# Optimization experiments

Measured on AMD Instinct MI355X. Metric: run time of the kernel, lower is better.

Reference implementation:

```python
import jax, jax.numpy as jnp
import numpy as np

B, S, D, H = 2, 2048, 1024, 16
DH = D // H  # head dim = 64


def _split_heads(x):
    # [B,S,D] -> [B,H,S,DH]
    return x.reshape(B, S, H, DH).transpose(0, 2, 1, 3)


def setup_inputs() -> dict:
    key = jax.random.key(0)
    ks = jax.random.split(key, 14)
    sc = 1.0 / np.sqrt(D)
    p = {"hidden_states": jax.random.normal(ks[0], (B, S, D), jnp.float32)}
    names = ["Wq", "Wk1", "Wk2", "Wv1", "Wv2", "Wd"]
    for i, n in enumerate(names):
        p[n] = jax.random.normal(ks[1 + 2 * i], (D, D), jnp.float32) * sc
        p["b" + n[1:]] = jax.random.normal(ks[2 + 2 * i], (D,), jnp.float32) * 0.02
    return p


def reference(hidden_states, Wq, bq, Wk1, bk1, Wk2, bk2, Wv1, bv1, Wv2, bv2, Wd, bd):
    q = _split_heads(hidden_states @ Wq + bq)
    k1 = _split_heads(hidden_states @ Wk1 + bk1)
    k2 = _split_heads(hidden_states @ Wk2 + bk2)
    v1 = _split_heads(hidden_states @ Wv1 + bv1)
    v2 = _split_heads(hidden_states @ Wv2 + bv2)

    scores = jnp.einsum("bhqd,bhkd->bhqk", q, k1) / np.sqrt(DH)
    causal = jnp.tril(jnp.ones((S, S), dtype=bool))  # True = keep
    scores = jnp.where(causal, scores, -jnp.inf)
    probs = jax.nn.softmax(scores, axis=-1)

    ctx = jnp.einsum("bhqk,bhkd->bhqd", probs, v1)          # [B,H,S,DH]
    ctx = jnp.einsum("bhqd,bhkd->bhqk", ctx, k2)            # [B,H,S,S]
    ctx = jnp.einsum("bhqk,bhkd->bhqd", ctx, v2)            # [B,H,S,DH]

    ctx = ctx.transpose(0, 2, 1, 3).reshape(B, S, D)
    return ctx @ Wd + bd
```

## Files before the change

### kernel.cpp

```cpp
#include <hip/hip_runtime.h>
#include <hip/hip_bf16.h>

typedef __bf16 bf16x8 __attribute__((ext_vector_type(8)));
typedef float f32x4 __attribute__((ext_vector_type(4)));
using bf16 = __hip_bfloat16;

#define SEQ 2048
#define DM 1024
#define NH 16
#define DH 64
#define NBH 32
#define MR 4096

#define WAITBAR(N) asm volatile("s_waitcnt vmcnt(" #N ")\n\ts_barrier" ::: "memory")

static __device__ __forceinline__ void async_cp16(const void* gsrc, void* ldsdst) {
  __builtin_amdgcn_global_load_lds((__attribute__((address_space(1))) void*)gsrc,
                                   (__attribute__((address_space(3))) void*)ldsdst, 16, 0, 0);
}

static __device__ __forceinline__ unsigned short f2bfu(float f) {
  bf16 h = __float2bfloat16(f);
  unsigned short u; __builtin_memcpy(&u, &h, 2); return u;
}
static __device__ __forceinline__ unsigned int pack_bf2(float lo, float hi) {
  return (unsigned int)f2bfu(lo) | ((unsigned int)f2bfu(hi) << 16);
}

struct WPtrs { const float* w[6]; };

__global__ __launch_bounds__(256) void prep(WPtrs wp, const float* __restrict__ X,
                                            bf16* __restrict__ WtAll, bf16* __restrict__ Xb,
                                            float* __restrict__ Mb) {
  __shared__ float Ts[32][33];
  const int z = blockIdx.z;
  const int tid = threadIdx.x;
  if (z < 6) {
    const float* W = wp.w[z];
    bf16* Wt = WtAll + (long)z * DM * DM;
    const int n0 = blockIdx.x * 32, k0 = blockIdx.y * 32;
    const int tx = tid & 31, ty = tid >> 5;
#pragma unroll
    for (int it = 0; it < 4; ++it)
      Ts[ty + 8 * it][tx] = W[(long)(k0 + ty + 8 * it) * DM + n0 + tx];
    __syncthreads();
#pragma unroll
    for (int it = 0; it < 4; ++it)
      Wt[(long)(n0 + ty + 8 * it) * DM + k0 + tx] = __float2bfloat16(Ts[tx][ty + 8 * it]);
    if (z == 0 && tid < 32) {
      int lin = blockIdx.x + 32 * blockIdx.y;
      f32x4 zz = {0.f, 0.f, 0.f, 0.f};
      *(f32x4*)(Mb + lin * 128 + tid * 4) = zz;
    }
  } else {
    int lin = blockIdx.x + 32 * blockIdx.y + (z - 6) * 1024;
    long g = (long)lin * 2048 + tid * 8;
    float4 a = *(const float4*)(X + g);
    float4 b = *(const float4*)(X + g + 4);
    unsigned short u[8];
    u[0]=f2bfu(a.x); u[1]=f2bfu(a.y); u[2]=f2bfu(a.z); u[3]=f2bfu(a.w);
    u[4]=f2bfu(b.x); u[5]=f2bfu(b.y); u[6]=f2bfu(b.z); u[7]=f2bfu(b.w);
    uint4 o; __builtin_memcpy(&o, u, 16);
    *(uint4*)(Xb + g) = o;
  }
}

struct ProjArgs {
  const float* bias[5];
  bf16* out[5];
};

__global__ __launch_bounds__(256, 2) void gemm_proj(const bf16* __restrict__ A,
                                                    const bf16* __restrict__ WtAll, ProjArgs p) {
  __shared__ alignas(16) bf16 SM[36864];
  bf16* As = SM;
  bf16* Bs = SM + 12288;
  const int tid = threadIdx.x;
  const int bid = blockIdx.x;
  const int wave = tid >> 6, lane = tid & 63, l15 = lane & 15, l4 = lane >> 4;
  const int wm = wave >> 1, wn = wave & 1;
  const int slot8 = (l4 ^ ((l15 >> 1) & 3)) * 8;
  const int prow = tid >> 2;
  const int cc = (tid & 3) ^ ((prow >> 1) & 3);
  char* dA = (char*)As + wave * 1024;
  char* dB = (char*)Bs + wave * 1024;

  if (bid < 512) {
    const int mt = bid & 31, nt = bid >> 5;
    const int m0 = mt * 128;
    const int z = nt >> 2;
    const int n0z = (nt & 3) * 256;
    const bf16* Bt = WtAll + (long)z * DM * DM + (long)n0z * DM;

    const bf16* sA0 = A  + (long)(m0 + prow) * DM + cc * 8;
    const bf16* sA1 = sA0 + 64L * DM;
    const bf16* sB0 = Bt + (long)prow * DM + cc * 8;
    const bf16* sB1 = sB0 + 64L * DM;
    const bf16* sB2 = sB0 + 128L * DM;
    const bf16* sB3 = sB0 + 192L * DM;

#define PSTAGE(KT_, BUF_) do {                                  \
    int ko_ = (KT_) * 32;                                       \
    async_cp16(sA0 + ko_, dA + (BUF_) * 8192);                  \
    async_cp16(sA1 + ko_, dA + (BUF_) * 8192 + 4096);           \
    async_cp16(sB0 + ko_, dB + (BUF_) * 16384);                 \
    async_cp16(sB1 + ko_, dB + (BUF_) * 16384 + 4096);          \
    async_cp16(sB2 + ko_, dB + (BUF_) * 16384 + 8192);          \
    async_cp16(sB3 + ko_, dB + (BUF_) * 16384 + 12288);         \
  } while (0)

    const int arow = wm * 64 + l15;
    const int brow = wn * 128 + l15;
    f32x4 acc[4][8] = {};

#define PCOMPUTE(BUF_) do {                                                        \
    const bf16* ab_ = As + (BUF_) * 4096;                                          \
    const bf16* bb_ = Bs + (BUF_) * 8192;                                          \
    bf16x8 af_[4], bq_[8];                                                         \
    _Pragma("unroll")                                                              \
    for (int i = 0; i < 4; ++i) af_[i] = *(const bf16x8*)(ab_ + (arow + i * 16) * 32 + slot8); \
    _Pragma("unroll")                                                              \
    for (int j = 0; j < 8; ++j) bq_[j] = *(const bf16x8*)(bb_ + (brow + j * 16) * 32 + slot8); \
    _Pragma("unroll")                                                              \
    for (int i = 0; i < 4; ++i)                                                    \
      _Pragma("unroll")                                                            \
      for (int j = 0; j < 8; ++j)                                                  \
        acc[i][j] = __builtin_amdgcn_mfma_f32_16x16x32_bf16(af_[i], bq_[j], acc[i][j], 0, 0, 0); \
  } while (0)

    PSTAGE(0, 0);
    PSTAGE(1, 1);
    int buf = 0;
#pragma unroll 1
    for (int k = 0; k < 31; ++k) {
      WAITBAR(6);
      if (k < 30) {
        int nb = buf + 2; if (nb > 2) nb -= 3;
        PSTAGE(k + 2, nb);
      }
      PCOMPUTE(buf);
      ++buf; if (buf > 2) buf = 0;
    }
    WAITBAR(0);
    PCOMPUTE(buf);
#undef PSTAGE
#undef PCOMPUTE

    const float* bias = p.bias[z];
    bf16* out = p.out[z];
    float bv[8];
#pragma unroll
    for (int j = 0; j < 8; ++j) bv[j] = bias[n0z + wn * 128 + j * 16 + l15];

    if (z < 2) {
      const float scale = (z == 0) ? 0.125f * 1.44269504f : 1.0f;
#pragma unroll
      for (int i = 0; i < 4; ++i)
#pragma unroll
        for (int j = 0; j < 8; ++j)
#pragma unroll
          for (int r = 0; r < 4; ++r) {
            int m = m0 + wm * 64 + i * 16 + l4 * 4 + r;
            int n = n0z + wn * 128 + j * 16 + l15;
            int b = m >> 11, s = m & 2047, hh = n >> 6, d = n & 63;
            out[((long)((b * NH + hh) * SEQ + s)) * DH + d] =
                __float2bfloat16((acc[i][j][r] + bv[j]) * scale);
          }
    } else {
      __syncthreads();
      bf16* Os = SM;
#pragma unroll
      for (int i = 0; i < 4; ++i)
#pragma unroll
        for (int j = 0; j < 8; ++j)
#pragma unroll
          for (int r = 0; r < 4; ++r) {
            int nl = wn * 128 + j * 16 + l15;
            int ml = wm * 64 + i * 16 + l4 * 4 + r;
            Os[nl * 136 + ml] = __float2bfloat16(acc[i][j][r] + bv[j]);
          }
      __syncthreads();
      {
        int nl = tid;
        int ng = n0z + nl;
        int hh = ng >> 6, d = ng & 63;
        int b = m0 >> 11, s0 = m0 & 2047;
        bf16* op = out + ((long)((b * NH + hh) * DH + d)) * SEQ + s0;
#pragma unroll
        for (int u = 0; u < 16; ++u)
          *(bf16x8*)(op + u * 8) = *(const bf16x8*)(Os + nl * 136 + u * 8);
      }
    }
  } else {
    const int tb = bid - 512;
    const int mt = tb & 31, nt16 = tb >> 5;
    const int m0 = mt * 128, n0 = nt16 * 64;
    const bf16* Bt = WtAll + 4L * DM * DM + (long)n0 * DM;

    const bf16* sA0 = A + (long)(m0 + prow) * DM + cc * 8;
    const bf16* sA1 = sA0 + 64L * DM;
    const bf16* sB0 = Bt + (long)prow * DM + cc * 8;

#define TSTAGE(KT_, BUF_) do {                                  \
    int ko_ = (KT_) * 32;                                       \
    async_cp16(sA0 + ko_, dA + (BUF_) * 8192);                  \
    async_cp16(sA1 + ko_, dA + (BUF_) * 8192 + 4096);           \
    async_cp16(sB0 + ko_, dB + (BUF_) * 4096);                  \
  } while (0)

    const int arow = wm * 64 + l15;
    const int brow = wn * 32 + l15;
    f32x4 acc2[4][2] = {};

#define TCOMPUTE(BUF_) do {                                                        \
    const bf16* ab_ = As + (BUF_) * 4096;                                          \
    const bf16* bb_ = Bs + (BUF_) * 2048;                                          \
    bf16x8 af_[4], bq_[2];                                                         \
    _Pragma("unroll")                                                              \
    for (int i = 0; i < 4; ++i) af_[i] = *(const bf16x8*)(ab_ + (arow + i * 16) * 32 + slot8); \
    _Pragma("unroll")                                                              \
    for (int j = 0; j < 2; ++j) bq_[j] = *(const bf16x8*)(bb_ + (brow + j * 16) * 32 + slot8); \
    _Pragma("unroll")                                                              \
    for (int i = 0; i < 4; ++i)                                                    \
      _Pragma("unroll")                                                            \
      for (int j = 0; j < 2; ++j)                                                  \
        acc2[i][j] = __builtin_amdgcn_mfma_f32_16x16x32_bf16(af_[i], bq_[j], acc2[i][j], 0, 0, 0); \
  } while (0)

    TSTAGE(0, 0);
    TSTAGE(1, 1);
    int buf = 0;
#pragma unroll 1
    for (int k = 0; k < 31; ++k) {
      WAITBAR(3);
      if (k < 30) {
        int nb = buf + 2; if (nb > 2) nb -= 3;
        TSTAGE(k + 2, nb);
      }
      TCOMPUTE(buf);
      ++buf; if (buf > 2) buf = 0;
    }
    WAITBAR(0);
    TCOMPUTE(buf);
#undef TSTAGE
#undef TCOMPUTE

    float bv2[2];
#pragma unroll
    for (int j = 0; j < 2; ++j) bv2[j] = p.bias[4][n0 + wn * 32 + j * 16 + l15];
    __syncthreads();
    bf16* Os = SM;
#pragma unroll
    for (int i = 0; i < 4; ++i)
#pragma unroll
      for (int j = 0; j < 2; ++j)
#pragma unroll
        for (int r = 0; r < 4; ++r) {
          int nl = wn * 32 + j * 16 + l15;
          int ml = wm * 64 + i * 16 + l4 * 4 + r;
          Os[nl * 136 + ml] = __float2bfloat16(acc2[i][j][r] + bv2[j]);
        }
    __syncthreads();
    {
      int nl = tid & 63, seg = tid >> 6;
      int ng = n0 + nl;
      int hh = ng >> 6, d = ng & 63;
      int b = m0 >> 11, s0 = m0 & 2047;
      bf16* op = p.out[4] + ((long)((b * NH + hh) * DH + d)) * SEQ + s0 + seg * 32;
#pragma unroll
      for (int u = 0; u < 4; ++u)
        *(bf16x8*)(op + u * 8) = *(const bf16x8*)(Os + nl * 136 + seg * 32 + u * 8);
    }
  }
}

__global__ __launch_bounds__(256, 3) void gemm_out(const bf16* __restrict__ A, const bf16* __restrict__ Bt,
                                                   const float* __restrict__ bias, float* __restrict__ out) {
  __shared__ alignas(16) bf16 As[3 * 128 * 32];
  __shared__ alignas(16) bf16 Bs[3 * 64 * 32];
  const int tid = threadIdx.x;
  const int bid = blockIdx.x;
  const int nt = bid & 15, mt = bid >> 4;
  const int m0 = mt * 128, n0 = nt * 64;
  const int wave = tid >> 6, lane = tid & 63, l15 = lane & 15, l4 = lane >> 4;
  const int wm = wave >> 1, wn = wave & 1;
  const int slot8 = (l4 ^ ((l15 >> 1) & 3)) * 8;
  const int prow = tid >> 2;
  const int cc = (tid & 3) ^ ((prow >> 1) & 3);
  const bf16* sA0 = A + (long)(m0 + prow) * DM + cc * 8;
  const bf16* sA1 = sA0 + 64L * DM;
  const bf16* sB0 = Bt + (long)(n0 + prow) * DM + cc * 8;
  char* dA = (char*)As + wave * 1024;
  char* dB = (char*)Bs + wave * 1024;

#define OSTAGE(KT_, BUF_) do {                                  \
    int ko_ = (KT_) * 32;                                       \
    async_cp16(sA0 + ko_, dA + (BUF_) * 8192);                  \
    async_cp16(sA1 + ko_, dA + (BUF_) * 8192 + 4096);           \
    async_cp16(sB0 + ko_, dB + (BUF_) * 4096);                  \
  } while (0)

  const int arow = wm * 64 + l15;
  const int brow = wn * 32 + l15;
  f32x4 acc2[4][2] = {};

#define OCOMPUTE(BUF_) do {                                                        \
    const bf16* ab_ = As + (BUF_) * 4096;                                          \
    const bf16* bb_ = Bs + (BUF_) * 2048;                                          \
    bf16x8 af_[4], bq_[2];                                                         \
    _Pragma("unroll")                                                              \
    for (int i = 0; i < 4; ++i) af_[i] = *(const bf16x8*)(ab_ + (arow + i * 16) * 32 + slot8); \
    _Pragma("unroll")                                                              \
    for (int j = 0; j < 2; ++j) bq_[j] = *(const bf16x8*)(bb_ + (brow + j * 16) * 32 + slot8); \
    _Pragma("unroll")                                                              \
    for (int i = 0; i < 4; ++i)                                                    \
      _Pragma("unroll")                                                            \
      for (int j = 0; j < 2; ++j)                                                  \
        acc2[i][j] = __builtin_amdgcn_mfma_f32_16x16x32_bf16(af_[i], bq_[j], acc2[i][j], 0, 0, 0); \
  } while (0)

  OSTAGE(0, 0);
  OSTAGE(1, 1);
  int buf = 0;
#pragma unroll 1
  for (int k = 0; k < 31; ++k) {
    WAITBAR(3);
    if (k < 30) {
      int nb = buf + 2; if (nb > 2) nb -= 3;
      OSTAGE(k + 2, nb);
    }
    OCOMPUTE(buf);
    ++buf; if (buf > 2) buf = 0;
  }
  WAITBAR(0);
  OCOMPUTE(buf);
#undef OSTAGE
#undef OCOMPUTE

  float bv[2];
#pragma unroll
  for (int j = 0; j < 2; ++j) bv[j] = bias[n0 + wn * 32 + j * 16 + l15];
#pragma unroll
  for (int i = 0; i < 4; ++i)
#pragma unroll
    for (int j = 0; j < 2; ++j)
#pragma unroll
      for (int r = 0; r < 4; ++r) {
        int m = m0 + wm * 64 + i * 16 + l4 * 4 + r;
        int n = n0 + wn * 32 + j * 16 + l15;
        out[(long)m * DM + n] = acc2[i][j][r] + bv[j];
      }
}

__global__ __launch_bounds__(256) void m_kernel(
    const bf16* __restrict__ k2t, const bf16* __restrict__ v2t, float* __restrict__ Mbuf)
{
  const int scx = blockIdx.x;
  const int bh = blockIdx.y;
  const int tid = threadIdx.x, wave = tid >> 6, lane = tid & 63, l15 = lane & 15, l4 = lane >> 4;
  const bf16* kp = k2t + (long)bh * DH * SEQ;
  const bf16* vp = v2t + (long)bh * DH * SEQ;
  __shared__ alignas(16) bf16 K2s[64 * 32];
  __shared__ alignas(16) bf16 V2s[64 * 32];
  f32x4 acc[4] = {};
  const int s0 = scx * 256;
  for (int kk = 0; kk < 256; kk += 32) {
    __syncthreads();
    {
      int c = tid, r = c >> 2, pp = c & 3;
      async_cp16(kp + (long)r * SEQ + s0 + kk + pp * 8, K2s + wave * 64 * 8);
      async_cp16(vp + (long)r * SEQ + s0 + kk + pp * 8, V2s + wave * 64 * 8);
    }
    __syncthreads();
    int arow = 16 * wave + l15;
    bf16x8 a = *(const bf16x8*)(K2s + arow * 32 + l4 * 8);
#pragma unroll
    for (int nb = 0; nb < 4; ++nb) {
      int col = nb * 16 + l15;
      bf16x8 b = *(const bf16x8*)(V2s + col * 32 + l4 * 8);
      acc[nb] = __builtin_amdgcn_mfma_f32_16x16x32_bf16(a, b, acc[nb], 0, 0, 0);
    }
  }
  float* Mp = Mbuf + (long)bh * 4096;
#pragma unroll
  for (int nb = 0; nb < 4; ++nb)
#pragma unroll
    for (int r = 0; r < 4; ++r) {
      int row = 16 * wave + l4 * 4 + r;
      int col = nb * 16 + l15;
      atomicAdd(Mp + row * 64 + col, acc[nb][r]);
    }
}

static __device__ __forceinline__ void redist(const unsigned int (&pk)[4][2], bf16x8 (&pb)[2],
                                              int l4, int l15) {
#pragma unroll
  for (int h = 0; h < 2; ++h) {
    unsigned int w4[4];
#pragma unroll
    for (int w = 0; w < 4; ++w) {
      int src = l15 + 16 * (2 * (l4 & 1) + (w >> 1));
      unsigned int va = (unsigned int)__shfl((int)pk[2 * h][w & 1], src);
      unsigned int vb = (unsigned int)__shfl((int)pk[2 * h + 1][w & 1], src);
      w4[w] = (l4 & 2) ? vb : va;
    }
    __builtin_memcpy(&pb[h], w4, 16);
  }
}

__global__ __launch_bounds__(256) void attn_fused(
    const bf16* __restrict__ q,
    const bf16* __restrict__ k1,
    const bf16* __restrict__ v1t,
    const float* __restrict__ Mbuf,
    bf16* __restrict__ ctx2)
{
  const int bid = blockIdx.x;
  const int xcd = bid & 7, ii = bid >> 3;
  const int bh = (xcd << 2) | (ii & 3);
  const int qpair = ii >> 2;
  const int bb = bh >> 4, hh = bh & 15;
  const int tid = threadIdx.x, wave = tid >> 6, lane = tid & 63;
  const int l15 = lane & 15, l4 = lane >> 4;
  const bf16* qp = q   + (long)bh * SEQ * DH;
  const bf16* kp = k1  + (long)bh * SEQ * DH;
  const bf16* vp = v1t + (long)bh * DH * SEQ;
  const float* Mp = Mbuf + (long)bh * 4096;

  __shared__ alignas(16) bf16 Ks[2][128 * 64];
  __shared__ alignas(16) bf16 Vs[2][64 * 128];

  bf16x8 mf[4][2];
#pragma unroll
  for (int db = 0; db < 4; ++db)
#pragma unroll
    for (int h = 0; h < 2; ++h) {
      bf16x8 t;
#pragma unroll
      for (int j = 0; j < 8; ++j)
        t[j] = (__bf16)Mp[(32 * h + 8 * l4 + j) * 64 + 16 * db + l15];
      mf[db][h] = t;
    }

#define STAGE_KV(JJ, BUF) do {                                                     \
    int kv0_ = 128 * (JJ);                                                         \
    int cK_ = (tid & 7) ^ ((tid >> 3) & 7);                                        \
    int cV_ = (tid & 15) ^ ((tid >> 4) & 15);                                      \
    _Pragma("unroll")                                                              \
    for (int p_ = 0; p_ < 4; ++p_) {                                               \
      int rK_ = (tid >> 3) + 32 * p_;                                              \
      async_cp16(kp + (long)(kv0_ + rK_) * DH + cK_ * 8,                           \
                 (char*)Ks[BUF] + p_ * 4096 + wave * 1024);                        \
      int rV_ = (tid >> 4) + 16 * p_;                                              \
      async_cp16(vp + (long)rV_ * SEQ + kv0_ + cV_ * 8,                            \
                 (char*)Vs[BUF] + p_ * 4096 + wave * 1024);                        \
    }                                                                              \
  } while (0)

#pragma unroll 1
  for (int half = 0; half < 2; ++half) {
    const int tq = (half == 0) ? (31 - qpair) : qpair;
    const int Q0 = 64 * tq;
    const int qg = Q0 + 16 * wave + l15;
    const int jm = tq >> 1;

    __syncthreads();
    STAGE_KV(0, 0);

    bf16x8 aq[2];
#pragma unroll
    for (int h = 0; h < 2; ++h)
      aq[h] = *(const bf16x8*)(qp + (long)qg * DH + 32 * h + 8 * l4);

    float m_run = -__builtin_inff(), l_run = 0.f;
    f32x4 acc_o[4] = {};

    __syncthreads();

#pragma unroll 1
    for (int j = 0; j <= jm; ++j) {
      const int cur = j & 1;
      if (j < jm) STAGE_KV(j + 1, cur ^ 1);

      f32x4 sc[8] = {};
      __builtin_amdgcn_s_setprio(1);
#pragma unroll
      for (int nb = 0; nb < 8; ++nb) {
        const bf16* krow = Ks[cur] + (16 * nb + l15) * 64;
#pragma unroll
        for (int h = 0; h < 2; ++h) {
          bf16x8 kf = *(const bf16x8*)(krow + (((4 * h + l4) ^ (l15 & 7)) * 8));
          sc[nb] = __builtin_amdgcn_mfma_f32_16x16x32_bf16(kf, aq[h], sc[nb], 0, 0, 0);
        }
      }
      __builtin_amdgcn_s_setprio(0);

      if (j == jm) {
        const int kv0 = 128 * j;
#pragma unroll
        for (int nb = 0; nb < 8; ++nb)
#pragma unroll
          for (int r = 0; r < 4; ++r)
            if (kv0 + 16 * nb + 4 * l4 + r > qg) sc[nb][r] = -__builtin_inff();
      }

      float tmax = -__builtin_inff();
#pragma unroll
      for (int nb = 0; nb < 8; ++nb)
#pragma unroll
        for (int r = 0; r < 4; ++r) tmax = fmaxf(tmax, sc[nb][r]);
      tmax = fmaxf(tmax, __shfl_xor(tmax, 16));
      tmax = fmaxf(tmax, __shfl_xor(tmax, 32));

      if (!__all(tmax <= m_run)) {
        float mnew = fmaxf(m_run, tmax);
        float sf = __builtin_amdgcn_exp2f(m_run - mnew);
        m_run = mnew;
        l_run *= sf;
#pragma unroll
        for (int db = 0; db < 4; ++db)
#pragma unroll
          for (int r = 0; r < 4; ++r) acc_o[db][r] *= sf;
      }

      float ssum = 0.f;
      unsigned int pkA[4][2], pkB[4][2];
#pragma unroll
      for (int nb = 0; nb < 4; ++nb)
#pragma unroll
        for (int pr = 0; pr < 2; ++pr) {
          float p0 = __builtin_amdgcn_exp2f(sc[nb][2 * pr]     - m_run);
          float p1 = __builtin_amdgcn_exp2f(sc[nb][2 * pr + 1] - m_run);
          ssum += p0 + p1;
          pkA[nb][pr] = pack_bf2(p0, p1);
        }
#pragma unroll
      for (int nb = 0; nb < 4; ++nb)
#pragma unroll
        for (int pr = 0; pr < 2; ++pr) {
          float p0 = __builtin_amdgcn_exp2f(sc[nb + 4][2 * pr]     - m_run);
          float p1 = __builtin_amdgcn_exp2f(sc[nb + 4][2 * pr + 1] - m_run);
          ssum += p0 + p1;
          pkB[nb][pr] = pack_bf2(p0, p1);
        }
      ssum += __shfl_xor(ssum, 16);
      ssum += __shfl_xor(ssum, 32);
      l_run += ssum;

      bf16x8 pbA[2], pbB[2];
      redist(pkA, pbA, l4, l15);
      redist(pkB, pbB, l4, l15);
      __builtin_amdgcn_s_setprio(1);
#pragma unroll
      for (int db = 0; db < 4; ++db) {
        const bf16* vrow = Vs[cur] + (16 * db + l15) * 128;
#pragma unroll
        for (int hs = 0; hs < 2; ++hs) {
          bf16x8 vf = *(const bf16x8*)(vrow + (((4 * hs + l4) ^ l15) * 8));
          acc_o[db] = __builtin_amdgcn_mfma_f32_16x16x32_bf16(vf, pbA[hs], acc_o[db], 0, 0, 0);
        }
#pragma unroll
        for (int hs = 0; hs < 2; ++hs) {
          bf16x8 vf = *(const bf16x8*)(vrow + (((4 * (hs + 2) + l4) ^ l15) * 8));
          acc_o[db] = __builtin_amdgcn_mfma_f32_16x16x32_bf16(vf, pbB[hs], acc_o[db], 0, 0, 0);
        }
      }
      __builtin_amdgcn_s_setprio(0);
      __syncthreads();
    }

    float invl = __builtin_amdgcn_rcpf(l_run);
    unsigned int ck[4][2];
#pragma unroll
    for (int db = 0; db < 4; ++db)
#pragma unroll
      for (int pr = 0; pr < 2; ++pr)
        ck[db][pr] = pack_bf2(acc_o[db][2 * pr] * invl, acc_o[db][2 * pr + 1] * invl);
    bf16x8 cb[2];
    redist(ck, cb, l4, l15);
    f32x4 o2[4] = {};
#pragma unroll
    for (int db = 0; db < 4; ++db)
#pragma unroll
      for (int h = 0; h < 2; ++h)
        o2[db] = __builtin_amdgcn_mfma_f32_16x16x32_bf16(mf[db][h], cb[h], o2[db], 0, 0, 0);

    bf16* Os = (bf16*)Ks;
#pragma unroll
    for (int db = 0; db < 4; ++db)
#pragma unroll
      for (int r = 0; r < 4; ++r)
        Os[(16 * wave + l15) * 72 + 16 * db + 4 * l4 + r] = __float2bfloat16(o2[db][r]);
    __syncthreads();
    {
      int rr = tid >> 2, cc2 = tid & 3;
      long obase = ((long)(bb * SEQ + Q0 + rr)) * DM + hh * DH + cc2 * 16;
      *(bf16x8*)(ctx2 + obase)     = *(const bf16x8*)(Os + rr * 72 + cc2 * 16);
      *(bf16x8*)(ctx2 + obase + 8) = *(const bf16x8*)(Os + rr * 72 + cc2 * 16 + 8);
    }
  }
#undef STAGE_KV
}

extern "C" void kernel_launch(void* const* d_in, const int* in_sizes, int n_in,
                              void* d_out, int out_size, void* d_ws, size_t ws_size,
                              hipStream_t stream) {
  (void)in_sizes; (void)n_in; (void)out_size; (void)ws_size;
  const float* X = (const float*)d_in[0];
  const float* W[6]    = {(const float*)d_in[1], (const float*)d_in[3], (const float*)d_in[5],
                          (const float*)d_in[7], (const float*)d_in[9], (const float*)d_in[11]};
  const float* bias[6] = {(const float*)d_in[2], (const float*)d_in[4], (const float*)d_in[6],
                          (const float*)d_in[8], (const float*)d_in[10], (const float*)d_in[12]};

  char* ws = (char*)d_ws;
  bf16* Xb  = (bf16*)(ws);
  bf16* Wt  = (bf16*)(ws + (8L  << 20));
  bf16* qB  = (bf16*)(ws + (20L << 20));
  bf16* k1B = (bf16*)(ws + (28L << 20));
  bf16* k2t = (bf16*)(ws + (36L << 20));
  bf16* v1t = (bf16*)(ws + (44L << 20));
  bf16* v2t = (bf16*)(ws + (52L << 20));
  float* Mb = (float*)(ws + (60L << 20));
  bf16* c2  = Xb;

  WPtrs wp; for (int z = 0; z < 6; ++z) wp.w[z] = W[z];
  prep<<<dim3(32, 32, 8), 256, 0, stream>>>(wp, X, Wt, Xb, Mb);

  ProjArgs pa;
  for (int z = 0; z < 5; ++z) pa.bias[z] = bias[z];
  pa.out[0] = qB; pa.out[1] = k1B; pa.out[2] = k2t; pa.out[3] = v1t; pa.out[4] = v2t;
  gemm_proj<<<1024, 256, 0, stream>>>(Xb, Wt, pa);

  m_kernel<<<dim3(8, 32), 256, 0, stream>>>(k2t, v2t, Mb);

  attn_fused<<<512, 256, 0, stream>>>(qB, k1B, v1t, Mb, c2);

  gemm_out<<<512, 256, 0, stream>>>(c2, Wt + 5L * DM * DM, bias[5], (float*)d_out);
}
```

Before: 142.0 us.

## Triple-buffer async LDS loads in m_kernel with 64-column chunks

Replaces the single-buffered load/sync/compute loop in m_kernel, which computes K2^T·V2 partial products, with a 3-stage ring of LDS buffers. Each stage loads 64 sequence columns, split into two 32-wide sub-blocks, and the loads are prefetched two chunks ahead. vmcnt-based waits plus a barrier replace the paired __syncthreads. The goal is to overlap global-to-LDS copies with MFMA work and halve the number of barriers, at the cost of more LDS per block (48KB vs 8KB), which may lower occupancy.

```diff
diff --git a/kernel.cpp b/kernel.cpp
--- a/kernel.cpp
+++ b/kernel.cpp
@@ -360,35 +360,57 @@
   const int tid = threadIdx.x, wave = tid >> 6, lane = tid & 63, l15 = lane & 15, l4 = lane >> 4;
   const bf16* kp = k2t + (long)bh * DH * SEQ;
   const bf16* vp = v2t + (long)bh * DH * SEQ;
-  __shared__ alignas(16) bf16 K2s[64 * 32];
-  __shared__ alignas(16) bf16 V2s[64 * 32];
+  __shared__ alignas(16) bf16 K2s[3][2][64 * 32];
+  __shared__ alignas(16) bf16 V2s[3][2][64 * 32];
   f32x4 acc[4] = {};
   const int s0 = scx * 256;
-  for (int kk = 0; kk < 256; kk += 32) {
-    __syncthreads();
-    {
-      int c = tid, r = c >> 2, pp = c & 3;
-      async_cp16(kp + (long)r * SEQ + s0 + kk + pp * 8, K2s + wave * 64 * 8);
-      async_cp16(vp + (long)r * SEQ + s0 + kk + pp * 8, V2s + wave * 64 * 8);
-    }
-    __syncthreads();
-    int arow = 16 * wave + l15;
-    bf16x8 a = *(const bf16x8*)(K2s + arow * 32 + l4 * 8);
-#pragma unroll
-    for (int nb = 0; nb < 4; ++nb) {
-      int col = nb * 16 + l15;
-      bf16x8 b = *(const bf16x8*)(V2s + col * 32 + l4 * 8);
-      acc[nb] = __builtin_amdgcn_mfma_f32_16x16x32_bf16(a, b, acc[nb], 0, 0, 0);
-    }
+  const int rr = tid >> 2, pp = tid & 3;
+  const bf16* kb = kp + (long)rr * SEQ + s0 + pp * 8;
+  const bf16* vb = vp + (long)rr * SEQ + s0 + pp * 8;
+
+#define MSTAGE(CH_, BUF_) do {                                            \
+    int co_ = (CH_) * 64;                                                 \
+    async_cp16(kb + co_,      (char*)K2s + (BUF_) * 8192 + wave * 1024);  \
+    async_cp16(kb + co_ + 32, (char*)K2s + (BUF_) * 8192 + 4096 + wave * 1024); \
+    async_cp16(vb + co_,      (char*)V2s + (BUF_) * 8192 + wave * 1024);  \
+    async_cp16(vb + co_ + 32, (char*)V2s + (BUF_) * 8192 + 4096 + wave * 1024); \
+  } while (0)
+
+  MSTAGE(0, 0);
+  MSTAGE(1, 1);
+  int buf = 0;
+  const int arow = 16 * wave + l15;
+#pragma unroll 1
+  for (int c = 0; c < 4; ++c) {
+    if (c == 3) { WAITBAR(0); } else { WAITBAR(4); }
+    if (c < 2) {
+      int nb = buf + 2; if (nb > 2) nb -= 3;
+      MSTAGE(c + 2, nb);
+    }
+#pragma unroll
+    for (int sb = 0; sb < 2; ++sb) {
+      const bf16* Kb = &K2s[buf][sb][0];
+      const bf16* Vb = &V2s[buf][sb][0];
+      bf16x8 a = *(const bf16x8*)(Kb + arow * 32 + l4 * 8);
+#pragma unroll
+      for (int nb2 = 0; nb2 < 4; ++nb2) {
+        int col = nb2 * 16 + l15;
+        bf16x8 b = *(const bf16x8*)(Vb + col * 32 + l4 * 8);
+        acc[nb2] = __builtin_amdgcn_mfma_f32_16x16x32_bf16(a, b, acc[nb2], 0, 0, 0);
+      }
+    }
+    ++buf; if (buf > 2) buf = 0;
   }
+#undef MSTAGE
+
   float* Mp = Mbuf + (long)bh * 4096;
 #pragma unroll
-  for (int nb = 0; nb < 4; ++nb)
+  for (int nb2 = 0; nb2 < 4; ++nb2)
 #pragma unroll
     for (int r = 0; r < 4; ++r) {
       int row = 16 * wave + l4 * 4 + r;
-      int col = nb * 16 + l15;
-      atomicAdd(Mp + row * 64 + col, acc[nb][r]);
+      int col = nb2 * 16 + l15;
+      atomicAdd(Mp + row * 64 + col, acc[nb2][r]);
     }
 }
 
```

Measured after the change: 141.6 us. Within noise of the previous version (-0.2%).
